# Kernel optimization log

Hardware: AMD Instinct MI355X
Metric: run time of the kernel (lower is better)

The kernel has to match this reference:

```python
import jax, jax.numpy as jnp
import numpy as np
import math

N_HEAD = 12
N_EMBD = 768

def setup_inputs() -> dict:
    key = jax.random.key(0)
    ks = jax.random.split(key, 5)
    B, T, C = 4, 2048, N_EMBD
    s_attn = 1.0 / math.sqrt(C)
    return {
        "x": jax.random.normal(ks[0], (B, T, C), jnp.float32),
        "w_attn": jax.random.normal(ks[1], (C, 3 * C), jnp.float32) * s_attn,
        "b_attn": jnp.zeros((3 * C,), jnp.float32),
        "w_proj": jax.random.normal(ks[2], (C, C), jnp.float32) * s_attn,
        "b_proj": jnp.zeros((C,), jnp.float32),
    }

def reference(x, w_attn, b_attn, w_proj, b_proj):
    B, T, C = x.shape
    H = N_HEAD
    D = C // H
    qkv = x @ w_attn + b_attn  # [B,T,3C]
    q, k, v = jnp.split(qkv, 3, axis=-1)
    # [B,T,C] -> [B,H,T,D]
    q = q.reshape(B, T, H, D).transpose(0, 2, 1, 3)
    k = k.reshape(B, T, H, D).transpose(0, 2, 1, 3)
    v = v.reshape(B, T, H, D).transpose(0, 2, 1, 3)
    att = jnp.einsum('bhqd,bhkd->bhqk', q, k) * (1.0 / math.sqrt(D))
    causal = jnp.tril(jnp.ones((T, T), bool))
    att = jnp.where(causal[None, None], att, -jnp.inf)
    att = jax.nn.softmax(att, axis=-1)
    y = jnp.einsum('bhqk,bhkd->bhqd', att, v)  # [B,H,T,D]
    y = y.transpose(0, 2, 1, 3).reshape(B, T, C)
    return y @ w_proj + b_proj
```

## Files before the change

### kernel.cpp

```cpp
#include <hip/hip_runtime.h>
#include <hip/hip_bf16.h>

typedef unsigned short u16;
typedef __attribute__((ext_vector_type(4))) short bf16x4;
typedef __attribute__((ext_vector_type(8))) short bf16x8;
typedef __attribute__((ext_vector_type(16))) float f32x16;

#define NB_ 4
#define NT_ 2048
#define NC_ 768
#define NH_ 12
#define ND_ 64
#define NM_ (NB_*NT_)
#define KC_ 24

#define SCQ_ 0.18033688011112042f

__device__ __forceinline__ u16 f2bf(float f){
  union { float f; unsigned u; } c; c.f = f;
  unsigned u = c.u;
  return (u16)((u + 0x7fffu + ((u>>16)&1u)) >> 16);
}

__device__ __forceinline__ unsigned pkbf(float a, float b){
  __hip_bfloat162 h = __float22bfloat162_rn(make_float2(a,b));
  union { __hip_bfloat162 h; unsigned u; } c; c.h = h; return c.u;
}

__device__ __forceinline__ f32x16 mfma32(bf16x8 a, bf16x8 b, f32x16 c){
  return __builtin_amdgcn_mfma_f32_32x32x16_bf16(a, b, c, 0, 0, 0);
}

__device__ __forceinline__ void gload_lds16(const void* g, void* l){
  __builtin_amdgcn_global_load_lds(
    (const __attribute__((address_space(1))) void*)g,
    (__attribute__((address_space(3))) void*)l, 16, 0, 0);
}


__global__ __launch_bounds__(256) void cast_f32_bf16_k(
    const float* __restrict__ in, u16* __restrict__ out, int n4){
  int i = blockIdx.x*256 + threadIdx.x;
  if (i >= n4) return;
  float4 v = ((const float4*)in)[i];
  int row = i / (NC_/4), k4 = (i % (NC_/4))*4;
  size_t off = (((size_t)(row>>7)*KC_ + (k4>>5))*4 + ((k4>>3)&3))*1024 + (row&127)*8 + (k4&7);
  bf16x4 o;
  o[0]=(short)f2bf(v.x); o[1]=(short)f2bf(v.y);
  o[2]=(short)f2bf(v.z); o[3]=(short)f2bf(v.w);
  *(bf16x4*)(out + off) = o;
}

template<int PAN>
__global__ __launch_bounds__(256) void transpose_cast_k(
    const float* __restrict__ in, u16* __restrict__ out, int R, int Cc){
  __shared__ float tile[32][33];
  int tx = threadIdx.x, ty = threadIdx.y;
  int c0 = blockIdx.x*32, r0 = blockIdx.y*32;
  #pragma unroll
  for (int j=0;j<32;j+=8) tile[ty+j][tx] = in[(size_t)(r0+ty+j)*Cc + c0+tx];
  __syncthreads();
  #pragma unroll
  for (int j=0;j<32;j+=8){
    int n = c0+ty+j, k = r0+tx;
    size_t off = ((size_t)(n/PAN)*KC_ + (k>>5))*(PAN*32)
               + (size_t)((k>>3)&3)*(PAN*8) + (n%PAN)*8 + (k&7);
    out[off] = f2bf(tile[tx][ty+j]);
  }
}

__global__ __launch_bounds__(256,3) void gemmQ(
  const u16* __restrict__ A, const u16* __restrict__ BT, const float* __restrict__ bias,
  u16* __restrict__ qo, u16* __restrict__ ko, u16* __restrict__ vo)
{
  __shared__ u16 lds[2][11264];
  const int t = threadIdx.x, w = t>>6, l = t&63;
  const int lq = l&31, h = l>>5;
  int sw = (blockIdx.x & 7)*96 + (blockIdx.x >> 3);
  const int rb = sw / 24, nb = sw % 24;
  const int brow = rb*256, bcol = nb*96;

  f32x16 acc[2][3];
  #pragma unroll
  for (int i=0;i<2;i++)
    #pragma unroll
    for (int j=0;j<3;j++)
      #pragma unroll
      for (int r=0;r<16;r++) acc[i][j][r] = 0.f;

  auto stage = [&](int buf, int kc){
    const u16* A0 = A  + ((size_t)((rb*2  )*KC_ + kc))*4096;
    const u16* A1 = A  + ((size_t)((rb*2+1)*KC_ + kc))*4096;
    const u16* Bg = BT + ((size_t)(nb*KC_ + kc))*3072;
    char* L = (char*)&lds[buf][0];
    gload_lds16(A0 + t*8,         L + t*16);
    gload_lds16(A0 + (256+t)*8,   L + (256+t)*16);
    gload_lds16(A1 + t*8,         L + 8192  + t*16);
    gload_lds16(A1 + (256+t)*8,   L + 8192  + (256+t)*16);
    gload_lds16(Bg + t*8,         L + 16384 + t*16);
    if (t < 128)
      gload_lds16(Bg + (256+t)*8, L + 16384 + (256+t)*16);
  };

  stage(0,0);
  int cur = 0;
  for (int kc=0; kc<KC_; ++kc){
    asm volatile("s_waitcnt vmcnt(0)\ns_barrier" ::: "memory");
    if (kc+1 < KC_) stage(cur^1, kc+1);
    const u16* La = &lds[cur][(w>>1)*4096];
    const u16* Lb = &lds[cur][8192];
    #pragma unroll
    for (int ks=0; ks<2; ++ks){
      bf16x8 af[2], bfr[3];
      #pragma unroll
      for (int mi=0;mi<2;mi++)
        af[mi]  = *(const bf16x8*)(La + ((2*ks+h)*128 + (w&1)*64 + mi*32 + lq)*8);
      #pragma unroll
      for (int nj=0;nj<3;nj++)
        bfr[nj] = *(const bf16x8*)(Lb + ((2*ks+h)*96 + nj*32 + lq)*8);
      __builtin_amdgcn_s_setprio(1);
      #pragma unroll
      for (int mi=0;mi<2;mi++)
        #pragma unroll
        for (int nj=0;nj<3;nj++)
          acc[mi][nj] = mfma32(af[mi], bfr[nj], acc[mi][nj]);
      __builtin_amdgcn_s_setprio(0);
    }
    cur ^= 1;
  }

  const int sec = nb >> 3;
  u16* outp = (sec==0) ? qo : (sec==1 ? ko : vo);
  #pragma unroll
  for (int nj=0;nj<3;nj++){
    int n = bcol + nj*32 + lq;
    int cc = n - sec*NC_;
    int hd = cc >> 6, d = cc & 63;
    float bs = bias[n];
    #pragma unroll
    for (int mi=0;mi<2;mi++)
      #pragma unroll
      for (int r=0;r<16;r++){
        int m = brow + w*64 + mi*32 + (r&3) + 8*(r>>2) + 4*h;
        int bb = m >> 11, tt = m & 2047;
        float v = acc[mi][nj][r] + bs;
        if (sec == 0) v *= SCQ_;
        size_t bhbase = ((size_t)bb*NH_ + hd)*((size_t)NT_*ND_);
        size_t off;
        if (sec == 0){
          off = bhbase + (size_t)tt*ND_ + d;
        } else if (sec == 1){
          off = bhbase + (size_t)(tt>>6)*4096 + (size_t)(d>>3)*512 + (tt&63)*8 + (d&7);
        } else {
          int p = (tt & ~15) | (h<<3) | (r&3) | (((r>>2)&1)<<2);
          off = bhbase + (size_t)(p>>6)*4096 + (size_t)((p&63)>>3)*512 + d*8 + (p&7);
        }
        outp[off] = f2bf(v);
      }
  }
}

__global__ __launch_bounds__(256,4) void gemmP(
  const u16* __restrict__ A, const u16* __restrict__ BT, const float* __restrict__ bias,
  float* __restrict__ fo)
{
  __shared__ u16 lds[2][8192];
  const int t = threadIdx.x, w = t>>6, l = t&63;
  const int lq = l&31, h = l>>5;
  int sw = (blockIdx.x & 7)*48 + (blockIdx.x >> 3);
  const int rb = sw / 6, nb = sw % 6;
  const int brow = rb*128, bcol = nb*128;
  const int wr = (w>>1)*64, wc = (w&1)*64;

  f32x16 acc[2][2];
  #pragma unroll
  for (int i=0;i<2;i++)
    #pragma unroll
    for (int j=0;j<2;j++)
      #pragma unroll
      for (int r=0;r<16;r++) acc[i][j][r] = 0.f;

  auto stage = [&](int buf, int kc){
    const u16* Ag = A  + ((size_t)(rb*KC_ + kc))*4096;
    const u16* Bg = BT + ((size_t)(nb*KC_ + kc))*4096;
    char* La = (char*)&lds[buf][0];
    char* Lb = (char*)&lds[buf][4096];
    #pragma unroll
    for (int it=0; it<2; ++it){
      gload_lds16(Ag + (it*256+t)*8, La + (it*256+t)*16);
      gload_lds16(Bg + (it*256+t)*8, Lb + (it*256+t)*16);
    }
  };

  stage(0,0);
  int cur = 0;
  for (int kc=0; kc<KC_; ++kc){
    asm volatile("s_waitcnt vmcnt(0)\ns_barrier" ::: "memory");
    if (kc+1 < KC_) stage(cur^1, kc+1);
    const u16* La = &lds[cur][0];
    const u16* Lb = &lds[cur][4096];
    #pragma unroll
    for (int ks=0; ks<2; ++ks){
      bf16x8 af[2], bfr[2];
      #pragma unroll
      for (int mi=0;mi<2;mi++)
        af[mi]  = *(const bf16x8*)(La + ((2*ks+h)*128 + wr + mi*32 + lq)*8);
      #pragma unroll
      for (int nj=0;nj<2;nj++)
        bfr[nj] = *(const bf16x8*)(Lb + ((2*ks+h)*128 + wc + nj*32 + lq)*8);
      __builtin_amdgcn_s_setprio(1);
      #pragma unroll
      for (int mi=0;mi<2;mi++)
        #pragma unroll
        for (int nj=0;nj<2;nj++)
          acc[mi][nj] = mfma32(af[mi], bfr[nj], acc[mi][nj]);
      __builtin_amdgcn_s_setprio(0);
    }
    cur ^= 1;
  }

  #pragma unroll
  for (int nj=0;nj<2;nj++){
    int n = bcol + wc + nj*32 + lq;
    float bs = bias[n];
    #pragma unroll
    for (int mi=0;mi<2;mi++)
      #pragma unroll
      for (int r=0;r<16;r++){
        int m = brow + wr + mi*32 + (r&3) + 8*(r>>2) + 4*h;
        fo[(size_t)m*NC_ + n] = acc[mi][nj][r] + bs;
      }
  }
}

__global__ __launch_bounds__(256,4) void attn_kernel(
    const u16* __restrict__ qg, const u16* __restrict__ kg,
    const u16* __restrict__ vg, u16* __restrict__ y)
{
  __shared__ u16 lds[2][8192];
  const int t = threadIdx.x, w = t>>6, l = t&63;
  const int lq = l&31, h = l>>5;
  const int bid = blockIdx.x;
  const int qt = 15 - (bid/48);
  const int bh = bid % 48;
  const int bb = bh / NH_, hh = bh % NH_;
  const u16* qp = qg + (size_t)bh*NT_*ND_;
  const u16* kp = kg + (size_t)bh*NT_*ND_;
  const u16* vp = vg + (size_t)bh*ND_*NT_;
  const int qmin = qt*128 + w*32;
  const int q = qmin + lq;

  bf16x8 Qf[4];
  {
    const u16* qr = qp + (size_t)q*ND_ + 8*h;
    #pragma unroll
    for (int ks=0; ks<4; ++ks) Qf[ks] = *(const bf16x8*)(qr + ks*16);
  }
  bf16x8 ones;
  #pragma unroll
  for (int i=0;i<8;i++) ones[i] = (short)0x3F80;

  f32x16 o0, o1, ls;
  #pragma unroll
  for (int r=0;r<16;r++){ o0[r]=0.f; o1[r]=0.f; ls[r]=0.f; }
  const int nc = 2*qt + 2;

  auto stage = [&](int buf, int c){
    const u16* kc2 = kp + c*4096;
    const u16* vc2 = vp + c*4096;
    #pragma unroll
    for (int it=0; it<2; ++it){
      gload_lds16(kc2 + (it*256 + t)*8, (char*)&lds[buf][0]    + (it*256 + t)*16);
      gload_lds16(vc2 + (it*256 + t)*8, (char*)&lds[buf][4096] + (it*256 + t)*16);
    }
  };

  stage(0,0);
  int cur = 0;
  for (int c=0; c<nc; ++c){
    asm volatile("s_waitcnt vmcnt(0)\ns_barrier" ::: "memory");
    if (c+1 < nc) stage(cur^1, c+1);

    const int kv0 = c*64;
    if (kv0 <= qmin + 31){
      const u16* Kb = &lds[cur][0];
      const u16* Vb = &lds[cur][4096];

      f32x16 s0, s1;
      #pragma unroll
      for (int r=0;r<16;r++){ s0[r]=0.f; s1[r]=0.f; }
      __builtin_amdgcn_s_setprio(1);
      #pragma unroll
      for (int ks=0; ks<4; ++ks){
        bf16x8 k0 = *(const bf16x8*)(Kb + ((2*ks+h)*64      + lq)*8);
        bf16x8 k1 = *(const bf16x8*)(Kb + ((2*ks+h)*64 + 32 + lq)*8);
        s0 = mfma32(k0, Qf[ks], s0);
        s1 = mfma32(k1, Qf[ks], s1);
      }
      __builtin_amdgcn_s_setprio(0);

      if (kv0 + 63 > qmin){
        #pragma unroll
        for (int r=0;r<16;r++){
          int kva = kv0 + (r&3) + 8*(r>>2) + 4*h;
          s0[r] = (kva      <= q) ? s0[r] : -3e38f;
          s1[r] = (kva + 32 <= q) ? s1[r] : -3e38f;
        }
      }

      union { unsigned wd[16]; bf16x8 v[4]; } pf;
      #pragma unroll
      for (int j=0;j<8;j++)
        pf.wd[j]   = pkbf(exp2f(s0[2*j]), exp2f(s0[2*j+1]));
      #pragma unroll
      for (int j=0;j<8;j++)
        pf.wd[8+j] = pkbf(exp2f(s1[2*j]), exp2f(s1[2*j+1]));

      __builtin_amdgcn_s_setprio(1);
      #pragma unroll
      for (int j=0;j<4;j++){
        bf16x8 v0 = *(const bf16x8*)(Vb + ((2*j+h)*64      + lq)*8);
        bf16x8 v1 = *(const bf16x8*)(Vb + ((2*j+h)*64 + 32 + lq)*8);
        o0 = mfma32(v0, pf.v[j], o0);
        o1 = mfma32(v1, pf.v[j], o1);
        ls = mfma32(ones, pf.v[j], ls);
      }
      __builtin_amdgcn_s_setprio(0);
    }
    cur ^= 1;
  }

  float inv = 1.f / ls[0];

  const int m = bb*NT_ + q;
  const int rbm = m>>7, rr = m&127;
  #pragma unroll
  for (int db=0; db<2; ++db){
    #pragma unroll
    for (int g2=0; g2<4; ++g2){
      float e0 = (db ? o1[g2*4+0] : o0[g2*4+0]) * inv;
      float e1 = (db ? o1[g2*4+1] : o0[g2*4+1]) * inv;
      float e2 = (db ? o1[g2*4+2] : o0[g2*4+2]) * inv;
      float e3 = (db ? o1[g2*4+3] : o0[g2*4+3]) * inv;
      unsigned w0 = pkbf(e0,e1), w1 = pkbf(e2,e3);
      int k = hh*ND_ + db*32 + g2*8 + 4*h;
      size_t off = (((size_t)rbm*KC_ + (k>>5))*4 + ((k>>3)&3))*1024 + rr*8 + (k&7);
      *(uint2*)(y + off) = make_uint2(w0, w1);
    }
  }
}

extern "C" void kernel_launch(void* const* d_in, const int* in_sizes, int n_in,
                              void* d_out, int out_size, void* d_ws, size_t ws_size,
                              hipStream_t stream) {
  const float* x  = (const float*)d_in[0];
  const float* wa = (const float*)d_in[1];
  const float* ba = (const float*)d_in[2];
  const float* wp = (const float*)d_in[3];
  const float* bp = (const float*)d_in[4];
  float* out = (float*)d_out;

  char* ws = (char*)d_ws;
  const size_t szXB = (size_t)NM_*NC_*2;
  const size_t szWA = (size_t)3*NC_*NC_*2;
  const size_t szWP = (size_t)NC_*NC_*2;
  const size_t szQ  = szXB;
  u16* xb  = (u16*)(ws);
  u16* wat = (u16*)(ws + szXB);
  u16* wpt = (u16*)(ws + szXB + szWA);
  u16* qb  = (u16*)(ws + szXB + szWA + szWP);
  u16* kb  = (u16*)((char*)qb + szQ);
  u16* vb  = (u16*)((char*)kb + szQ);
  u16* yb  = xb;

  cast_f32_bf16_k<<<dim3((NM_*NC_/4 + 255)/256), dim3(256), 0, stream>>>(x, xb, NM_*NC_/4);
  transpose_cast_k<96><<<dim3(3*NC_/32, NC_/32), dim3(32,8), 0, stream>>>(wa, wat, NC_, 3*NC_);
  transpose_cast_k<128><<<dim3(NC_/32, NC_/32), dim3(32,8), 0, stream>>>(wp, wpt, NC_, NC_);
  gemmQ<<<dim3(768), dim3(256), 0, stream>>>(xb, wat, ba, qb, kb, vb);
  attn_kernel<<<dim3(NB_*NH_*(NT_/128)), dim3(256), 0, stream>>>(qb, kb, vb, yb);
  gemmP<<<dim3(384), dim3(256), 0, stream>>>(yb, wpt, bp, out);
}
```

Baseline: 131.8 us.

## Enlarge attention KV chunk from 64 to 96 keys with matching K/V layout

```diff
diff --git a/kernel.cpp b/kernel.cpp
--- a/kernel.cpp
+++ b/kernel.cpp
@@ -13,6 +13,9 @@
 #define ND_ 64
 #define NM_ (NB_*NT_)
 #define KC_ 24
+#define NCH_ 22
+#define CHSZ_ 6144
+#define BHC_ (NCH_*CHSZ_)
 
 #define SCQ_ 0.18033688011112042f
 
@@ -145,15 +148,16 @@
         int bb = m >> 11, tt = m & 2047;
         float v = acc[mi][nj][r] + bs;
         if (sec == 0) v *= SCQ_;
-        size_t bhbase = ((size_t)bb*NH_ + hd)*((size_t)NT_*ND_);
         size_t off;
         if (sec == 0){
-          off = bhbase + (size_t)tt*ND_ + d;
+          off = ((size_t)bb*NH_ + hd)*((size_t)NT_*ND_) + (size_t)tt*ND_ + d;
         } else if (sec == 1){
-          off = bhbase + (size_t)(tt>>6)*4096 + (size_t)(d>>3)*512 + (tt&63)*8 + (d&7);
+          off = ((size_t)bb*NH_ + hd)*BHC_
+              + (size_t)(tt/96)*CHSZ_ + (size_t)(d>>3)*768 + (tt%96)*8 + (d&7);
         } else {
           int p = (tt & ~15) | (h<<3) | (r&3) | (((r>>2)&1)<<2);
-          off = bhbase + (size_t)(p>>6)*4096 + (size_t)((p&63)>>3)*512 + d*8 + (p&7);
+          off = ((size_t)bb*NH_ + hd)*BHC_
+              + (size_t)(p/96)*CHSZ_ + (size_t)((p%96)>>3)*512 + d*8 + (p&7);
         }
         outp[off] = f2bf(v);
       }
@@ -233,11 +237,11 @@
   }
 }
 
-__global__ __launch_bounds__(256,4) void attn_kernel(
+__global__ __launch_bounds__(256,3) void attn_kernel(
     const u16* __restrict__ qg, const u16* __restrict__ kg,
     const u16* __restrict__ vg, u16* __restrict__ y)
 {
-  __shared__ u16 lds[2][8192];
+  __shared__ u16 lds[2][12288];
   const int t = threadIdx.x, w = t>>6, l = t&63;
   const int lq = l&31, h = l>>5;
   const int bid = blockIdx.x;
@@ -245,8 +249,8 @@
   const int bh = bid % 48;
   const int bb = bh / NH_, hh = bh % NH_;
   const u16* qp = qg + (size_t)bh*NT_*ND_;
-  const u16* kp = kg + (size_t)bh*NT_*ND_;
-  const u16* vp = vg + (size_t)bh*ND_*NT_;
+  const u16* kp = kg + (size_t)bh*BHC_;
+  const u16* vp = vg + (size_t)bh*BHC_;
   const int qmin = qt*128 + w*32;
   const int q = qmin + lq;
 
@@ -263,15 +267,15 @@
   f32x16 o0, o1, ls;
   #pragma unroll
   for (int r=0;r<16;r++){ o0[r]=0.f; o1[r]=0.f; ls[r]=0.f; }
-  const int nc = 2*qt + 2;
+  const int nc = ((qt+1)*128 + 95)/96;
 
   auto stage = [&](int buf, int c){
-    const u16* kc2 = kp + c*4096;
-    const u16* vc2 = vp + c*4096;
-    #pragma unroll
-    for (int it=0; it<2; ++it){
+    const u16* kc2 = kp + (size_t)c*CHSZ_;
+    const u16* vc2 = vp + (size_t)c*CHSZ_;
+    #pragma unroll
+    for (int it=0; it<3; ++it){
       gload_lds16(kc2 + (it*256 + t)*8, (char*)&lds[buf][0]    + (it*256 + t)*16);
-      gload_lds16(vc2 + (it*256 + t)*8, (char*)&lds[buf][4096] + (it*256 + t)*16);
+      gload_lds16(vc2 + (it*256 + t)*8, (char*)&lds[buf][6144] + (it*256 + t)*16);
     }
   };
 
@@ -281,48 +285,51 @@
     asm volatile("s_waitcnt vmcnt(0)\ns_barrier" ::: "memory");
     if (c+1 < nc) stage(cur^1, c+1);
 
-    const int kv0 = c*64;
+    const int kv0 = c*96;
     if (kv0 <= qmin + 31){
       const u16* Kb = &lds[cur][0];
-      const u16* Vb = &lds[cur][4096];
-
-      f32x16 s0, s1;
-      #pragma unroll
-      for (int r=0;r<16;r++){ s0[r]=0.f; s1[r]=0.f; }
+      const u16* Vb = &lds[cur][6144];
+
+      f32x16 s0, s1, s2;
+      #pragma unroll
+      for (int r=0;r<16;r++){ s0[r]=0.f; s1[r]=0.f; s2[r]=0.f; }
       __builtin_amdgcn_s_setprio(1);
       #pragma unroll
       for (int ks=0; ks<4; ++ks){
-        bf16x8 k0 = *(const bf16x8*)(Kb + ((2*ks+h)*64      + lq)*8);
-        bf16x8 k1 = *(const bf16x8*)(Kb + ((2*ks+h)*64 + 32 + lq)*8);
-        s0 = mfma32(k0, Qf[ks], s0);
-        s1 = mfma32(k1, Qf[ks], s1);
+        const u16* kb0 = Kb + (2*ks+h)*768 + lq*8;
+        s0 = mfma32(*(const bf16x8*)(kb0),       Qf[ks], s0);
+        s1 = mfma32(*(const bf16x8*)(kb0 + 256), Qf[ks], s1);
+        s2 = mfma32(*(const bf16x8*)(kb0 + 512), Qf[ks], s2);
       }
       __builtin_amdgcn_s_setprio(0);
 
-      if (kv0 + 63 > qmin){
+      if (kv0 + 95 > qmin){
         #pragma unroll
         for (int r=0;r<16;r++){
           int kva = kv0 + (r&3) + 8*(r>>2) + 4*h;
           s0[r] = (kva      <= q) ? s0[r] : -3e38f;
           s1[r] = (kva + 32 <= q) ? s1[r] : -3e38f;
+          s2[r] = (kva + 64 <= q) ? s2[r] : -3e38f;
         }
       }
 
-      union { unsigned wd[16]; bf16x8 v[4]; } pf;
+      union { unsigned wd[24]; bf16x8 v[6]; } pf;
       #pragma unroll
       for (int j=0;j<8;j++)
-        pf.wd[j]   = pkbf(exp2f(s0[2*j]), exp2f(s0[2*j+1]));
+        pf.wd[j]    = pkbf(exp2f(s0[2*j]), exp2f(s0[2*j+1]));
       #pragma unroll
       for (int j=0;j<8;j++)
-        pf.wd[8+j] = pkbf(exp2f(s1[2*j]), exp2f(s1[2*j+1]));
+        pf.wd[8+j]  = pkbf(exp2f(s1[2*j]), exp2f(s1[2*j+1]));
+      #pragma unroll
+      for (int j=0;j<8;j++)
+        pf.wd[16+j] = pkbf(exp2f(s2[2*j]), exp2f(s2[2*j+1]));
 
       __builtin_amdgcn_s_setprio(1);
       #pragma unroll
-      for (int j=0;j<4;j++){
-        bf16x8 v0 = *(const bf16x8*)(Vb + ((2*j+h)*64      + lq)*8);
-        bf16x8 v1 = *(const bf16x8*)(Vb + ((2*j+h)*64 + 32 + lq)*8);
-        o0 = mfma32(v0, pf.v[j], o0);
-        o1 = mfma32(v1, pf.v[j], o1);
+      for (int j=0;j<6;j++){
+        const u16* vb0 = Vb + (2*j+h)*512 + lq*8;
+        o0 = mfma32(*(const bf16x8*)(vb0),       pf.v[j], o0);
+        o1 = mfma32(*(const bf16x8*)(vb0 + 256), pf.v[j], o1);
         ls = mfma32(ones, pf.v[j], ls);
       }
       __builtin_amdgcn_s_setprio(0);
@@ -363,14 +370,13 @@
   char* ws = (char*)d_ws;
   const size_t szXB = (size_t)NM_*NC_*2;
   const size_t szWA = (size_t)3*NC_*NC_*2;
-  const size_t szWP = (size_t)NC_*NC_*2;
-  const size_t szQ  = szXB;
+  const size_t szKV = (size_t)48*BHC_*2;
   u16* xb  = (u16*)(ws);
-  u16* wat = (u16*)(ws + szXB);
-  u16* wpt = (u16*)(ws + szXB + szWA);
-  u16* qb  = (u16*)(ws + szXB + szWA + szWP);
-  u16* kb  = (u16*)((char*)qb + szQ);
-  u16* vb  = (u16*)((char*)kb + szQ);
+  u16* qb  = (u16*)(ws + szXB);
+  u16* kb  = (u16*)((char*)qb + szXB);
+  u16* vb  = (u16*)((char*)kb + szKV);
+  u16* wat = (u16*)((char*)vb + szKV);
+  u16* wpt = (u16*)((char*)wat + szWA);
   u16* yb  = xb;
 
   cast_f32_bf16_k<<<dim3((NM_*NC_/4 + 255)/256), dim3(256), 0, stream>>>(x, xb, NM_*NC_/4);
```

New measurement: 132.4 us. No clear change (+0.5%).

## Process two 32-row query tiles per wave in attention, halving block threads

Applied to the files above, without the earlier changes.

```diff
diff --git a/kernel.cpp b/kernel.cpp
--- a/kernel.cpp
+++ b/kernel.cpp
@@ -233,7 +233,7 @@
   }
 }
 
-__global__ __launch_bounds__(256,4) void attn_kernel(
+__global__ __launch_bounds__(128,2) void attn_kernel(
     const u16* __restrict__ qg, const u16* __restrict__ kg,
     const u16* __restrict__ vg, u16* __restrict__ y)
 {
@@ -246,32 +246,33 @@
   const int bb = bh / NH_, hh = bh % NH_;
   const u16* qp = qg + (size_t)bh*NT_*ND_;
   const u16* kp = kg + (size_t)bh*NT_*ND_;
-  const u16* vp = vg + (size_t)bh*ND_*NT_;
-  const int qmin = qt*128 + w*32;
-  const int q = qmin + lq;
-
-  bf16x8 Qf[4];
-  {
-    const u16* qr = qp + (size_t)q*ND_ + 8*h;
-    #pragma unroll
-    for (int ks=0; ks<4; ++ks) Qf[ks] = *(const bf16x8*)(qr + ks*16);
+  const u16* vp = vg + (size_t)bh*NT_*ND_;
+  const int qmw = qt*128 + w*64;
+
+  bf16x8 Qf[2][4];
+  #pragma unroll
+  for (int j=0;j<2;j++){
+    const u16* qr = qp + (size_t)(qmw + j*32 + lq)*ND_ + 8*h;
+    #pragma unroll
+    for (int ks=0; ks<4; ++ks) Qf[j][ks] = *(const bf16x8*)(qr + ks*16);
   }
   bf16x8 ones;
   #pragma unroll
   for (int i=0;i<8;i++) ones[i] = (short)0x3F80;
 
-  f32x16 o0, o1, ls;
-  #pragma unroll
-  for (int r=0;r<16;r++){ o0[r]=0.f; o1[r]=0.f; ls[r]=0.f; }
+  f32x16 o00, o01, o10, o11, ls0, ls1;
+  #pragma unroll
+  for (int r=0;r<16;r++){ o00[r]=0.f; o01[r]=0.f; o10[r]=0.f; o11[r]=0.f;
+                          ls0[r]=0.f; ls1[r]=0.f; }
   const int nc = 2*qt + 2;
 
   auto stage = [&](int buf, int c){
     const u16* kc2 = kp + c*4096;
     const u16* vc2 = vp + c*4096;
     #pragma unroll
-    for (int it=0; it<2; ++it){
-      gload_lds16(kc2 + (it*256 + t)*8, (char*)&lds[buf][0]    + (it*256 + t)*16);
-      gload_lds16(vc2 + (it*256 + t)*8, (char*)&lds[buf][4096] + (it*256 + t)*16);
+    for (int it=0; it<4; ++it){
+      gload_lds16(kc2 + (it*128 + t)*8, (char*)&lds[buf][0]    + (it*128 + t)*16);
+      gload_lds16(vc2 + (it*128 + t)*8, (char*)&lds[buf][4096] + (it*128 + t)*16);
     }
   };
 
@@ -282,70 +283,88 @@
     if (c+1 < nc) stage(cur^1, c+1);
 
     const int kv0 = c*64;
-    if (kv0 <= qmin + 31){
+    if (kv0 <= qmw + 63){
       const u16* Kb = &lds[cur][0];
       const u16* Vb = &lds[cur][4096];
 
-      f32x16 s0, s1;
-      #pragma unroll
-      for (int r=0;r<16;r++){ s0[r]=0.f; s1[r]=0.f; }
+      bf16x8 kf[8];
+      #pragma unroll
+      for (int ks=0; ks<4; ++ks){
+        kf[2*ks]   = *(const bf16x8*)(Kb + ((2*ks+h)*64      + lq)*8);
+        kf[2*ks+1] = *(const bf16x8*)(Kb + ((2*ks+h)*64 + 32 + lq)*8);
+      }
+
+      union { unsigned wd[16]; bf16x8 v[4]; } pf[2];
+      #pragma unroll
+      for (int j=0;j<2;j++){
+        f32x16 s0, s1;
+        #pragma unroll
+        for (int r=0;r<16;r++){ s0[r]=0.f; s1[r]=0.f; }
+        __builtin_amdgcn_s_setprio(1);
+        #pragma unroll
+        for (int ks=0; ks<4; ++ks){
+          s0 = mfma32(kf[2*ks],   Qf[j][ks], s0);
+          s1 = mfma32(kf[2*ks+1], Qf[j][ks], s1);
+        }
+        __builtin_amdgcn_s_setprio(0);
+
+        if (kv0 + 63 > qmw + j*32){
+          int qj = qmw + j*32 + lq;
+          #pragma unroll
+          for (int r=0;r<16;r++){
+            int kva = kv0 + (r&3) + 8*(r>>2) + 4*h;
+            s0[r] = (kva      <= qj) ? s0[r] : -3e38f;
+            s1[r] = (kva + 32 <= qj) ? s1[r] : -3e38f;
+          }
+        }
+        #pragma unroll
+        for (int jj=0;jj<8;jj++)
+          pf[j].wd[jj]   = pkbf(exp2f(s0[2*jj]), exp2f(s0[2*jj+1]));
+        #pragma unroll
+        for (int jj=0;jj<8;jj++)
+          pf[j].wd[8+jj] = pkbf(exp2f(s1[2*jj]), exp2f(s1[2*jj+1]));
+      }
+
+      bf16x8 vf[8];
+      #pragma unroll
+      for (int jj=0;jj<4;jj++){
+        vf[2*jj]   = *(const bf16x8*)(Vb + ((2*jj+h)*64      + lq)*8);
+        vf[2*jj+1] = *(const bf16x8*)(Vb + ((2*jj+h)*64 + 32 + lq)*8);
+      }
       __builtin_amdgcn_s_setprio(1);
       #pragma unroll
-      for (int ks=0; ks<4; ++ks){
-        bf16x8 k0 = *(const bf16x8*)(Kb + ((2*ks+h)*64      + lq)*8);
-        bf16x8 k1 = *(const bf16x8*)(Kb + ((2*ks+h)*64 + 32 + lq)*8);
-        s0 = mfma32(k0, Qf[ks], s0);
-        s1 = mfma32(k1, Qf[ks], s1);
+      for (int jj=0;jj<4;jj++){
+        o00 = mfma32(vf[2*jj],   pf[0].v[jj], o00);
+        o01 = mfma32(vf[2*jj+1], pf[0].v[jj], o01);
+        ls0 = mfma32(ones,       pf[0].v[jj], ls0);
+        o10 = mfma32(vf[2*jj],   pf[1].v[jj], o10);
+        o11 = mfma32(vf[2*jj+1], pf[1].v[jj], o11);
+        ls1 = mfma32(ones,       pf[1].v[jj], ls1);
       }
       __builtin_amdgcn_s_setprio(0);
-
-      if (kv0 + 63 > qmin){
-        #pragma unroll
-        for (int r=0;r<16;r++){
-          int kva = kv0 + (r&3) + 8*(r>>2) + 4*h;
-          s0[r] = (kva      <= q) ? s0[r] : -3e38f;
-          s1[r] = (kva + 32 <= q) ? s1[r] : -3e38f;
-        }
-      }
-
-      union { unsigned wd[16]; bf16x8 v[4]; } pf;
-      #pragma unroll
-      for (int j=0;j<8;j++)
-        pf.wd[j]   = pkbf(exp2f(s0[2*j]), exp2f(s0[2*j+1]));
-      #pragma unroll
-      for (int j=0;j<8;j++)
-        pf.wd[8+j] = pkbf(exp2f(s1[2*j]), exp2f(s1[2*j+1]));
-
-      __builtin_amdgcn_s_setprio(1);
-      #pragma unroll
-      for (int j=0;j<4;j++){
-        bf16x8 v0 = *(const bf16x8*)(Vb + ((2*j+h)*64      + lq)*8);
-        bf16x8 v1 = *(const bf16x8*)(Vb + ((2*j+h)*64 + 32 + lq)*8);
-        o0 = mfma32(v0, pf.v[j], o0);
-        o1 = mfma32(v1, pf.v[j], o1);
-        ls = mfma32(ones, pf.v[j], ls);
-      }
-      __builtin_amdgcn_s_setprio(0);
     }
     cur ^= 1;
   }
 
-  float inv = 1.f / ls[0];
-
-  const int m = bb*NT_ + q;
-  const int rbm = m>>7, rr = m&127;
-  #pragma unroll
-  for (int db=0; db<2; ++db){
-    #pragma unroll
-    for (int g2=0; g2<4; ++g2){
-      float e0 = (db ? o1[g2*4+0] : o0[g2*4+0]) * inv;
-      float e1 = (db ? o1[g2*4+1] : o0[g2*4+1]) * inv;
-      float e2 = (db ? o1[g2*4+2] : o0[g2*4+2]) * inv;
-      float e3 = (db ? o1[g2*4+3] : o0[g2*4+3]) * inv;
-      unsigned w0 = pkbf(e0,e1), w1 = pkbf(e2,e3);
-      int k = hh*ND_ + db*32 + g2*8 + 4*h;
-      size_t off = (((size_t)rbm*KC_ + (k>>5))*4 + ((k>>3)&3))*1024 + rr*8 + (k&7);
-      *(uint2*)(y + off) = make_uint2(w0, w1);
+  #pragma unroll
+  for (int j=0;j<2;j++){
+    float inv = 1.f / (j ? ls1[0] : ls0[0]);
+    const int m = bb*NT_ + qmw + j*32 + lq;
+    const int rbm = m>>7, rr = m&127;
+    #pragma unroll
+    for (int db=0; db<2; ++db){
+      const f32x16& ov = j ? (db ? o11 : o10) : (db ? o01 : o00);
+      #pragma unroll
+      for (int g2=0; g2<4; ++g2){
+        float e0 = ov[g2*4+0] * inv;
+        float e1 = ov[g2*4+1] * inv;
+        float e2 = ov[g2*4+2] * inv;
+        float e3 = ov[g2*4+3] * inv;
+        unsigned w0 = pkbf(e0,e1), w1 = pkbf(e2,e3);
+        int k = hh*ND_ + db*32 + g2*8 + 4*h;
+        size_t off = (((size_t)rbm*KC_ + (k>>5))*4 + ((k>>3)&3))*1024 + rr*8 + (k&7);
+        *(uint2*)(y + off) = make_uint2(w0, w1);
+      }
     }
   }
 }
@@ -377,6 +396,6 @@
   transpose_cast_k<96><<<dim3(3*NC_/32, NC_/32), dim3(32,8), 0, stream>>>(wa, wat, NC_, 3*NC_);
   transpose_cast_k<128><<<dim3(NC_/32, NC_/32), dim3(32,8), 0, stream>>>(wp, wpt, NC_, NC_);
   gemmQ<<<dim3(768), dim3(256), 0, stream>>>(xb, wat, ba, qb, kb, vb);
-  attn_kernel<<<dim3(NB_*NH_*(NT_/128)), dim3(256), 0, stream>>>(qb, kb, vb, yb);
+  attn_kernel<<<dim3(NB_*NH_*(NT_/128)), dim3(128), 0, stream>>>(qb, kb, vb, yb);
   gemmP<<<dim3(384), dim3(256), 0, stream>>>(yb, wpt, bp, out);
 }
```

After: 176.0 us. 1.34x slower.

## Split attention KV range across two blocks and combine partials

Applied to the files above, without the earlier changes.

```diff
diff --git a/kernel.cpp b/kernel.cpp
--- a/kernel.cpp
+++ b/kernel.cpp
@@ -25,6 +25,10 @@
 __device__ __forceinline__ unsigned pkbf(float a, float b){
   __hip_bfloat162 h = __float22bfloat162_rn(make_float2(a,b));
   union { __hip_bfloat162 h; unsigned u; } c; c.h = h; return c.u;
+}
+
+__device__ __forceinline__ float bf2f(short s){
+  union { unsigned u; float f; } c; c.u = ((unsigned)(u16)s) << 16; return c.f;
 }
 
 __device__ __forceinline__ f32x16 mfma32(bf16x8 a, bf16x8 b, f32x16 c){
@@ -233,20 +237,22 @@
   }
 }
 
-__global__ __launch_bounds__(256,4) void attn_kernel(
+__global__ __launch_bounds__(256,5) void attn_kernel(
     const u16* __restrict__ qg, const u16* __restrict__ kg,
-    const u16* __restrict__ vg, u16* __restrict__ y)
+    const u16* __restrict__ vg, u16* __restrict__ pa, u16* __restrict__ pb2,
+    float* __restrict__ la, float* __restrict__ lb)
 {
   __shared__ u16 lds[2][8192];
   const int t = threadIdx.x, w = t>>6, l = t&63;
   const int lq = l&31, h = l>>5;
   const int bid = blockIdx.x;
-  const int qt = 15 - (bid/48);
-  const int bh = bid % 48;
+  const int qt = 15 - (bid/96);
+  const int half = bid & 1;
+  const int bh = (bid % 96) >> 1;
   const int bb = bh / NH_, hh = bh % NH_;
   const u16* qp = qg + (size_t)bh*NT_*ND_;
   const u16* kp = kg + (size_t)bh*NT_*ND_;
-  const u16* vp = vg + (size_t)bh*ND_*NT_;
+  const u16* vp = vg + (size_t)bh*NT_*ND_;
   const int qmin = qt*128 + w*32;
   const int q = qmin + lq;
 
@@ -263,7 +269,8 @@
   f32x16 o0, o1, ls;
   #pragma unroll
   for (int r=0;r<16;r++){ o0[r]=0.f; o1[r]=0.f; ls[r]=0.f; }
-  const int nc = 2*qt + 2;
+  const int c0 = half ? (qt+1) : 0;
+  const int c1 = half ? (2*qt+2) : (qt+1);
 
   auto stage = [&](int buf, int c){
     const u16* kc2 = kp + c*4096;
@@ -275,11 +282,11 @@
     }
   };
 
-  stage(0,0);
+  stage(0, c0);
   int cur = 0;
-  for (int c=0; c<nc; ++c){
+  for (int c=c0; c<c1; ++c){
     asm volatile("s_waitcnt vmcnt(0)\ns_barrier" ::: "memory");
-    if (c+1 < nc) stage(cur^1, c+1);
+    if (c+1 < c1) stage(cur^1, c+1);
 
     const int kv0 = c*64;
     if (kv0 <= qmin + 31){
@@ -330,24 +337,51 @@
     cur ^= 1;
   }
 
-  float inv = 1.f / ls[0];
-
+  u16* po = half ? pb2 : pa;
+  float* lo = half ? lb : la;
   const int m = bb*NT_ + q;
   const int rbm = m>>7, rr = m&127;
   #pragma unroll
   for (int db=0; db<2; ++db){
     #pragma unroll
     for (int g2=0; g2<4; ++g2){
-      float e0 = (db ? o1[g2*4+0] : o0[g2*4+0]) * inv;
-      float e1 = (db ? o1[g2*4+1] : o0[g2*4+1]) * inv;
-      float e2 = (db ? o1[g2*4+2] : o0[g2*4+2]) * inv;
-      float e3 = (db ? o1[g2*4+3] : o0[g2*4+3]) * inv;
+      float e0 = (db ? o1[g2*4+0] : o0[g2*4+0]);
+      float e1 = (db ? o1[g2*4+1] : o0[g2*4+1]);
+      float e2 = (db ? o1[g2*4+2] : o0[g2*4+2]);
+      float e3 = (db ? o1[g2*4+3] : o0[g2*4+3]);
       unsigned w0 = pkbf(e0,e1), w1 = pkbf(e2,e3);
       int k = hh*ND_ + db*32 + g2*8 + 4*h;
       size_t off = (((size_t)rbm*KC_ + (k>>5))*4 + ((k>>3)&3))*1024 + rr*8 + (k&7);
-      *(uint2*)(y + off) = make_uint2(w0, w1);
-    }
-  }
+      *(uint2*)(po + off) = make_uint2(w0, w1);
+    }
+  }
+  if (h == 0) lo[(size_t)bh*NT_ + q] = ls[0];
+}
+
+__global__ __launch_bounds__(256) void combine_k(
+    u16* __restrict__ pa, const u16* __restrict__ pb2,
+    const float* __restrict__ la, const float* __restrict__ lb)
+{
+  size_t i = (size_t)blockIdx.x*256 + threadIdx.x;
+  size_t f = i*8;
+  bf16x8 a = *(const bf16x8*)(pa + f);
+  bf16x8 b = *(const bf16x8*)(pb2 + f);
+  int grp = (int)(f >> 10);
+  int rr  = ((int)f & 1023) >> 3;
+  int rbm = grp / 96, rem = grp % 96;
+  int k   = (rem>>2)*32 + (rem&3)*8;
+  int m   = rbm*128 + rr;
+  int bh  = (m>>11)*NH_ + (k>>6);
+  int q   = m & 2047;
+  float inv = 1.f / (la[(size_t)bh*NT_ + q] + lb[(size_t)bh*NT_ + q]);
+  unsigned wd[4];
+  #pragma unroll
+  for (int j=0;j<4;j++){
+    float e0 = (bf2f(a[2*j])   + bf2f(b[2*j]))   * inv;
+    float e1 = (bf2f(a[2*j+1]) + bf2f(b[2*j+1])) * inv;
+    wd[j] = pkbf(e0, e1);
+  }
+  *(uint4*)(pa + f) = make_uint4(wd[0], wd[1], wd[2], wd[3]);
 }
 
 extern "C" void kernel_launch(void* const* d_in, const int* in_sizes, int n_in,
@@ -365,18 +399,23 @@
   const size_t szWA = (size_t)3*NC_*NC_*2;
   const size_t szWP = (size_t)NC_*NC_*2;
   const size_t szQ  = szXB;
+  const size_t szLS = (size_t)48*NT_*4;
   u16* xb  = (u16*)(ws);
   u16* wat = (u16*)(ws + szXB);
   u16* wpt = (u16*)(ws + szXB + szWA);
   u16* qb  = (u16*)(ws + szXB + szWA + szWP);
   u16* kb  = (u16*)((char*)qb + szQ);
   u16* vb  = (u16*)((char*)kb + szQ);
-  u16* yb  = xb;
+  float* la = (float*)((char*)vb + szQ);
+  float* lb = (float*)((char*)la + szLS);
+  u16* pa  = xb;
+  u16* pb2 = (u16*)d_out;
 
   cast_f32_bf16_k<<<dim3((NM_*NC_/4 + 255)/256), dim3(256), 0, stream>>>(x, xb, NM_*NC_/4);
   transpose_cast_k<96><<<dim3(3*NC_/32, NC_/32), dim3(32,8), 0, stream>>>(wa, wat, NC_, 3*NC_);
   transpose_cast_k<128><<<dim3(NC_/32, NC_/32), dim3(32,8), 0, stream>>>(wp, wpt, NC_, NC_);
   gemmQ<<<dim3(768), dim3(256), 0, stream>>>(xb, wat, ba, qb, kb, vb);
-  attn_kernel<<<dim3(NB_*NH_*(NT_/128)), dim3(256), 0, stream>>>(qb, kb, vb, yb);
-  gemmP<<<dim3(384), dim3(256), 0, stream>>>(yb, wpt, bp, out);
-}
+  attn_kernel<<<dim3(1536), dim3(256), 0, stream>>>(qb, kb, vb, pa, pb2, la, lb);
+  combine_k<<<dim3((NM_*NC_/8)/256), dim3(256), 0, stream>>>(pa, pb2, la, lb);
+  gemmP<<<dim3(384), dim3(256), 0, stream>>>(pa, wpt, bp, out);
+}
```

Measured after the change: 205.9 us. 1.56x slower.
